# Kernel tuning notes

Measured on AMD Instinct MI355X. Metric: run time of the kernel, lower is better.

## Reference

```python
import jax, jax.numpy as jnp
import numpy as np

C_IN = 512


def _rms(h, gamma):
    # F.normalize(x, dim=1) * sqrt(C) * gamma  (channel_first, h: [b, c, l])
    c = h.shape[1]
    n = jnp.sqrt(jnp.sum(h * h, axis=1, keepdims=True))
    return h / jnp.maximum(n, 1e-12) * (c ** 0.5) * gamma[None, :, None]


def _pw(w, b, h):
    # 1x1 conv == pointwise linear over channel dim; h: [b, c, l]
    return jnp.einsum('oc,bcl->bol', w, h) + b[None, :, None]


def setup_inputs() -> dict:
    key = jax.random.key(0)
    ks = jax.random.split(key, 10)
    B, C, T, H, W = 1, C_IN, 16, 32, 32
    inp = {'x': jax.random.normal(ks[0], (B, C, T, H, W), jnp.float32)}
    names = ['qs', 'ks', 'vs', 'ps', 'qt', 'kt', 'vt', 'pt']
    for i, n in enumerate(names):
        inp[n + '_w'] = jax.random.normal(ks[i + 1], (C, C), jnp.float32) * 0.02
        inp[n + '_b'] = jnp.zeros((C,), jnp.float32)
    inp['norm_s_gamma'] = jnp.ones((C,), jnp.float32)
    inp['norm_t_gamma'] = jnp.ones((C,), jnp.float32)
    inp['max_temporal_window'] = 8
    return inp


def reference(x, qs_w, qs_b, ks_w, ks_b, vs_w, vs_b, ps_w, ps_b,
              qt_w, qt_b, kt_w, kt_b, vt_w, vt_b, pt_w, pt_b,
              norm_s_gamma, norm_t_gamma, max_temporal_window):
    B, C, T, H, W = x.shape
    scale = C ** -0.5

    # ---- spatial attention: (b t) c (h w) ----
    xs = x.transpose(0, 2, 1, 3, 4).reshape(B * T, C, H * W)
    h = _rms(xs, norm_s_gamma)
    q = _pw(qs_w, qs_b, h)
    k = _pw(ks_w, ks_b, h)
    v = _pw(vs_w, vs_b, h)
    scores = jnp.einsum('bcl,bcm->blm', q, k) * scale  # [bt, HW, HW]
    attn = jax.nn.softmax(scores, axis=-1)
    o = jnp.einsum('bcm,blm->bcl', v, attn)
    xs = xs + _pw(ps_w, ps_b, o)
    x = xs.reshape(B, T, C, H, W).transpose(0, 2, 1, 3, 4)

    # ---- temporal attention: (b h w) c t, causal + bounded window ----
    xt = x.transpose(0, 3, 4, 1, 2).reshape(B * H * W, C, T)
    h = _rms(xt, norm_t_gamma)
    q = _pw(qt_w, qt_b, h)
    k = _pw(kt_w, kt_b, h)
    v = _pw(vt_w, vt_b, h)
    scores = jnp.einsum('bcl,bcm->blm', q, k) * scale  # [bhw, T, T]
    i = jnp.arange(T)[:, None]
    j = jnp.arange(T)[None, :]
    allowed = j <= i  # causal
    if max_temporal_window is not None and max_temporal_window > 0:
        allowed = allowed & (i - j < max_temporal_window)  # sliding window
    mask = jnp.where(allowed, 0.0, jnp.finfo(scores.dtype).min)
    attn = jax.nn.softmax(scores + mask[None], axis=-1)
    o = jnp.einsum('bcm,blm->bcl', v, attn)
    xt = xt + _pw(pt_w, pt_b, o)
    x = xt.reshape(B, H, W, C, T).transpose(0, 3, 4, 1, 2)
    return x
```

## Files before the change

### kernel.cpp

```cpp
#include <hip/hip_runtime.h>

typedef __attribute__((ext_vector_type(8))) short bf16x8;
typedef __attribute__((ext_vector_type(4))) float f32x4;

__device__ __forceinline__ short f2bf(float f) {
  union { float f; unsigned u; } a; a.f = f;
  unsigned r = a.u + 0x7fffu + ((a.u >> 16) & 1u);
  return (short)(r >> 16);
}
__device__ __forceinline__ float bf2f(short s) {
  union { unsigned u; float f; } a;
  a.u = ((unsigned)(unsigned short)s) << 16; return a.f;
}
__device__ __forceinline__ float blo(unsigned u) { union { unsigned u; float f; } a; a.u = u << 16; return a.f; }
__device__ __forceinline__ float bhi(unsigned u) { union { unsigned u; float f; } a; a.u = u & 0xffff0000u; return a.f; }
__device__ __forceinline__ unsigned packbf(float lo, float hi) {
  return (unsigned)(unsigned short)f2bf(lo) | ((unsigned)(unsigned short)f2bf(hi) << 16);
}
__device__ __forceinline__ void ldscp16(const void* g, void* l) {
  __builtin_amdgcn_global_load_lds((const __attribute__((address_space(1))) void*)g,
                                   (__attribute__((address_space(3))) void*)l, 16, 0, 0);
}
__device__ __forceinline__ void stv(float* p, float v) { *p = v; }
__device__ __forceinline__ void stv(short* p, float v) { *p = f2bf(v); }

__global__ __launch_bounds__(256) void setup_all(
    const float* __restrict__ w0, const float* __restrict__ w1,
    const float* __restrict__ w2, const float* __restrict__ w3,
    const float* __restrict__ w4, const float* __restrict__ w5,
    const float* __restrict__ w6, const float* __restrict__ w7,
    const float* __restrict__ g_s, const float* __restrict__ g_t,
    short* __restrict__ Wb,
    const float* __restrict__ b0, const float* __restrict__ b1,
    const float* __restrict__ b2, const float* __restrict__ b3,
    const float* __restrict__ b4, const float* __restrict__ b5,
    const float* __restrict__ b6, const float* __restrict__ b7,
    float* __restrict__ Ball, float* __restrict__ zs,
    const float* __restrict__ ps_w, const float* __restrict__ vs_b,
    const float* __restrict__ ps_b, const float* __restrict__ pt_w,
    const float* __restrict__ vt_b, const float* __restrict__ pt_b,
    float* __restrict__ bt_s, float* __restrict__ bt_t) {
  const int bid = blockIdx.x, tid = threadIdx.x;
  if (bid < 8192) {
    int idx = bid * 256 + tid;
    const float* ws[8] = {w0, w1, w2, w3, w4, w5, w6, w7};
    int wi = idx >> 18, loc = idx & 262143;
    int r = loc >> 9, q = loc & 511;
    float v, g;
    if (wi == 2 || wi == 6) {
      v = ws[wi][q * 512 + r];
      g = (wi == 2) ? g_s[r] : g_t[r];
    } else {
      v = ws[wi][loc];
      g = (wi <= 1) ? g_s[q] : (wi == 4 || wi == 5) ? g_t[q] : 1.f;
    }
    Wb[idx] = f2bf(v * g);
  } else if (bid < 8384) {
    zs[(bid - 8192) * 256 + tid] = 0.f;
  } else if (bid < 8400) {
    int idx = (bid - 8384) * 256 + tid;
    const float* bs[8] = {b0, b1, b2, b3, b4, b5, b6, b7};
    Ball[idx] = bs[idx >> 9][idx & 511];
  } else {
    const int w = tid >> 6, lane = tid & 63;
    const int b = (bid - 8400) * 4 + w;
    const bool sp = b < 512;
    const float* W = sp ? ps_w : pt_w;
    const float* vb = sp ? vs_b : vt_b;
    const float* pb = sp ? ps_b : pt_b;
    float* o = sp ? bt_s : bt_t;
    const int r = b & 511;
    float s = 0.f;
#pragma unroll
    for (int c = lane; c < 512; c += 64) s += W[r * 512 + c] * vb[c];
#pragma unroll
    for (int off = 32; off > 0; off >>= 1) s += __shfl_xor(s, off);
    if (lane == 0) o[r] = s + pb[r];
  }
}

__global__ __launch_bounds__(256) void txp_sumsq(
    const float* __restrict__ src, short* __restrict__ dst,
    short* __restrict__ xb, float* __restrict__ ss) {
  constexpr long N = 16384;
  __shared__ short T[64][66];
  __shared__ float part[16][16][4];
  const int tid = threadIdx.x;
  const long n0 = (long)blockIdx.x * 64;
  const int c0 = blockIdx.y * 64;
  const int n4 = (tid & 15) * 4;
  float s0 = 0.f, s1 = 0.f, s2 = 0.f, s3 = 0.f;
#pragma unroll
  for (int i = 0; i < 4; ++i) {
    int cl = i * 16 + (tid >> 4);
    float4 v = *(const float4*)&src[(long)(c0 + cl) * N + n0 + n4];
    s0 += v.x * v.x; s1 += v.y * v.y; s2 += v.z * v.z; s3 += v.w * v.w;
    short e0 = f2bf(v.x), e1 = f2bf(v.y), e2 = f2bf(v.z), e3 = f2bf(v.w);
    T[n4 + 0][cl] = e0; T[n4 + 1][cl] = e1;
    T[n4 + 2][cl] = e2; T[n4 + 3][cl] = e3;
    uint2 o;
    o.x = (unsigned)(unsigned short)e0 | ((unsigned)(unsigned short)e1 << 16);
    o.y = (unsigned)(unsigned short)e2 | ((unsigned)(unsigned short)e3 << 16);
    *(uint2*)&xb[(long)(c0 + cl) * N + n0 + n4] = o;
  }
  part[tid >> 4][tid & 15][0] = s0; part[tid >> 4][tid & 15][1] = s1;
  part[tid >> 4][tid & 15][2] = s2; part[tid >> 4][tid & 15][3] = s3;
  __syncthreads();
  if (tid < 64) {
    float s = 0.f;
#pragma unroll
    for (int cg = 0; cg < 16; ++cg) s += part[cg][tid >> 2][tid & 3];
    atomicAdd(&ss[n0 + tid], s);
  }
#pragma unroll
  for (int p = 0; p < 4; ++p) {
    int nl = p * 16 + (tid >> 4);
    int cl = (tid & 15) * 4;
    uint2 o;
    o.x = (unsigned)(unsigned short)T[nl][cl] |
          ((unsigned)(unsigned short)T[nl][cl + 1] << 16);
    o.y = (unsigned)(unsigned short)T[nl][cl + 2] |
          ((unsigned)(unsigned short)T[nl][cl + 3] << 16);
    *(uint2*)&dst[(n0 + nl) * 512 + c0 + cl] = o;
  }
}

template <typename OutT, int BIAS_MODE, int SCALE_MODE, int RESID_MODE, int EPI>
__global__ __launch_bounds__(256, 3) void gemm_nt(
    const short* __restrict__ A, const short* __restrict__ B,
    OutT* __restrict__ D, const float* __restrict__ bias,
    const float* __restrict__ ssv, float* __restrict__ rs,
    const float* __restrict__ residf, const short* __restrict__ residb,
    int K, int lda, int ldb, int ldd,
    long aBatch, long bBatch, long dBatch, long sBatch, float scale) {
  __shared__ short As[128 * 64];
  __shared__ short Bs[128 * 64];
  const int tid = threadIdx.x;
  const int bz = blockIdx.z;
  const long i0 = (long)blockIdx.x * 128;
  const long j0 = (long)blockIdx.y * 128;
  const short* Ab = A + bz * aBatch + i0 * lda;
  const short* Bb = B + bz * bBatch + j0 * ldb;
  const int srow = tid >> 3, scol = tid & 7;
  const int lane = tid & 63;
  const int wr = ((tid >> 7) & 1) * 64;
  const int wc = ((tid >> 6) & 1) * 64;
  const int quad = lane >> 4, l15 = lane & 15;

  f32x4 acc[4][4] = {};

  for (int k0 = 0; k0 < K; k0 += 64) {
    __syncthreads();
#pragma unroll
    for (int p = 0; p < 4; ++p) {
      int row = p * 32 + srow;
      int gc = (scol ^ (row & 7)) << 3;
      ldscp16(Ab + (long)row * lda + k0 + gc, &As[p * 2048 + tid * 8]);
    }
#pragma unroll
    for (int p = 0; p < 4; ++p) {
      int row = p * 32 + srow;
      int gc = (scol ^ (row & 7)) << 3;
      ldscp16(Bb + (long)row * ldb + k0 + gc, &Bs[p * 2048 + tid * 8]);
    }
    __syncthreads();
#pragma unroll
    for (int kk = 0; kk < 2; ++kk) {
      bf16x8 af[4], bfr[4];
#pragma unroll
      for (int a = 0; a < 4; ++a) {
        int row = wr + a * 16 + l15;
        int g = kk * 4 + quad;
        af[a] = *(const bf16x8*)&As[row * 64 + ((g ^ (row & 7)) << 3)];
      }
#pragma unroll
      for (int b = 0; b < 4; ++b) {
        int row = wc + b * 16 + l15;
        int g = kk * 4 + quad;
        bfr[b] = *(const bf16x8*)&Bs[row * 64 + ((g ^ (row & 7)) << 3)];
      }
#pragma unroll
      for (int a = 0; a < 4; ++a)
#pragma unroll
        for (int b = 0; b < 4; ++b)
          acc[a][b] = __builtin_amdgcn_mfma_f32_16x16x32_bf16(af[a], bfr[b], acc[a][b], 0, 0, 0);
    }
  }

  const long Doff = bz * dBatch;
#pragma unroll
  for (int a = 0; a < 4; ++a) {
    const int rb = (int)i0 + wr + a * 16 + quad * 4;
    float rsc[4];
    if (SCALE_MODE == 1) {
#pragma unroll
      for (int r = 0; r < 4; ++r)
        rsc[r] = 22.627416997969522f /
                 fmaxf(sqrtf(ssv[bz * sBatch + rb + r]), 1e-12f);
    }
    if (SCALE_MODE == 3) {
#pragma unroll
      for (int r = 0; r < 4; ++r)
        rsc[r] = 1.f / ssv[bz * sBatch + rb + r];
    }
    float rowpart[4] = {0.f, 0.f, 0.f, 0.f};
#pragma unroll
    for (int b = 0; b < 4; ++b) {
      const int cc = (int)j0 + wc + b * 16 + l15;
      float csc = 1.f;
      if (SCALE_MODE == 2)
        csc = 22.627416997969522f /
              fmaxf(sqrtf(ssv[bz * sBatch + cc]), 1e-12f);
      uint2 rtv;
      if (RESID_MODE == 3)
        rtv = *(const uint2*)&residb[(long)cc * 512 + rb];
#pragma unroll
      for (int r = 0; r < 4; ++r) {
        float val = acc[a][b][r] * scale;
        if (EPI == 1) { val = __expf(val); rowpart[r] += val; }
        if (SCALE_MODE == 1 || SCALE_MODE == 3) val *= rsc[r];
        if (SCALE_MODE == 2) val *= csc;
        if (BIAS_MODE == 1) val += bias[rb + r];
        if (BIAS_MODE == 2) val += bias[cc];
        const long off = Doff + (long)(rb + r) * ldd + cc;
        if (RESID_MODE == 1) val += residf[off];
        if (RESID_MODE == 2) val += bf2f(residb[off]);
        if (RESID_MODE == 3) val += bf2f(((const short*)&rtv)[r]);
        stv(D + off, val);
        if (EPI == 2) rowpart[r] += val * val;
      }
    }
    if (EPI) {
#pragma unroll
      for (int r = 0; r < 4; ++r) {
        float s = rowpart[r];
#pragma unroll
        for (int off = 1; off < 16; off <<= 1) s += __shfl_xor(s, off);
        if (l15 == 0) atomicAdd(&rs[bz * sBatch + rb + r], s);
      }
    }
  }
}

__global__ __launch_bounds__(256) void temporal_attn_v4(
    const short* __restrict__ qk, const short* __restrict__ h2,
    const float* __restrict__ ss, const int* __restrict__ wndp,
    short* __restrict__ o, float scale) {
  constexpr int RS = 1032;
  __shared__ short qs[16 * RS];
  __shared__ float Plds[16][17];
  const int tid = threadIdx.x;
  const int w = tid >> 6, lane = tid & 63;
  const int hw = blockIdx.x;
  const int wnd = *wndp;

#pragma unroll
  for (int i = 0; i < 8; ++i) {
    int ci = w * 8 + i;
    int t = ci >> 1, half = ci & 1;
    ldscp16(qk + (long)(t * 1024 + hw) * 1024 + half * 512 + lane * 8,
            &qs[t * RS + half * 512 + lane * 8]);
  }
  const int c0 = lane * 8;
  uint4 vch[16];
#pragma unroll
  for (int tp = 0; tp < 16; ++tp)
    vch[tp] = *(const uint4*)(h2 + (long)(tp * 1024 + hw) * 512 + c0);
  __syncthreads();

  if (w == 0) {
    const int quad = lane >> 4, m = lane & 15;
    const short* rowp = &qs[m * RS + quad * 8];
    f32x4 sacc = {};
#pragma unroll
    for (int s = 0; s < 16; ++s) {
      bf16x8 aq = *(const bf16x8*)(rowp + s * 32);
      bf16x8 bk = *(const bf16x8*)(rowp + 512 + s * 32);
      sacc = __builtin_amdgcn_mfma_f32_16x16x32_bf16(aq, bk, sacc, 0, 0, 0);
    }
    const float rmsm = 22.627416997969522f /
                       fmaxf(sqrtf(ss[m * 1024 + hw]), 1e-12f);
#pragma unroll
    for (int r = 0; r < 4; ++r) {
      const int i = quad * 4 + r;
      const int j = m;
      const bool allowed = (j <= i) && (wnd <= 0 || (i - j) < wnd);
      float val = allowed ? sacc[r] * scale : -1e30f;
      float mx = val;
#pragma unroll
      for (int off = 1; off < 16; off <<= 1) mx = fmaxf(mx, __shfl_xor(mx, off));
      float e = allowed ? __expf(val - mx) : 0.f;
      float sum = e;
#pragma unroll
      for (int off = 1; off < 16; off <<= 1) sum += __shfl_xor(sum, off);
      Plds[i][j] = (e / sum) * rmsm;
    }
  }
  __syncthreads();

#pragma unroll
  for (int r = 0; r < 4; ++r) {
    const int t = w * 4 + r;
    const int tlo = (wnd > 0 && t - wnd + 1 > 0) ? t - wnd + 1 : 0;
    float a0 = 0.f, a1 = 0.f, a2 = 0.f, a3 = 0.f,
          a4 = 0.f, a5 = 0.f, a6 = 0.f, a7 = 0.f;
#pragma unroll
    for (int tp = 0; tp < 16; ++tp) {
      const float p = (tp >= tlo && tp <= t) ? Plds[t][tp] : 0.f;
      const uint4 vv = vch[tp];
      a0 += p * blo(vv.x); a1 += p * bhi(vv.x);
      a2 += p * blo(vv.y); a3 += p * bhi(vv.y);
      a4 += p * blo(vv.z); a5 += p * bhi(vv.z);
      a6 += p * blo(vv.w); a7 += p * bhi(vv.w);
    }
    uint4 ov;
    ov.x = packbf(a0, a1); ov.y = packbf(a2, a3);
    ov.z = packbf(a4, a5); ov.w = packbf(a6, a7);
    *(uint4*)(o + (long)(t * 1024 + hw) * 512 + c0) = ov;
  }
}

extern "C" void kernel_launch(void* const* d_in, const int* in_sizes, int n_in,
                              void* d_out, int out_size, void* d_ws, size_t ws_size,
                              hipStream_t stream) {
  const float* x    = (const float*)d_in[0];
  const float* qs_w = (const float*)d_in[1];
  const float* qs_b = (const float*)d_in[2];
  const float* ks_w = (const float*)d_in[3];
  const float* ks_b = (const float*)d_in[4];
  const float* vs_w = (const float*)d_in[5];
  const float* vs_b = (const float*)d_in[6];
  const float* ps_w = (const float*)d_in[7];
  const float* ps_b = (const float*)d_in[8];
  const float* qt_w = (const float*)d_in[9];
  const float* qt_b = (const float*)d_in[10];
  const float* kt_w = (const float*)d_in[11];
  const float* kt_b = (const float*)d_in[12];
  const float* vt_w = (const float*)d_in[13];
  const float* vt_b = (const float*)d_in[14];
  const float* pt_w = (const float*)d_in[15];
  const float* pt_b = (const float*)d_in[16];
  const float* g_s  = (const float*)d_in[17];
  const float* g_t  = (const float*)d_in[18];
  const int*   wnd  = (const int*)d_in[19];
  float* out = (float*)d_out;

  char* w = (char*)d_ws;
  short* Wb   = (short*)(w);
  float* Ball = (float*)(w + (4L << 20));
  float* ss_s = (float*)(w + (4L << 20) + (64 << 10));
  float* ss_t = (float*)(w + (4L << 20) + (128 << 10));
  float* rsum = (float*)(w + (4L << 20) + (192 << 10));
  float* bt_s = (float*)(w + (4L << 20) + (256 << 10));
  float* bt_t = (float*)(w + (4L << 20) + (260 << 10));
  short* Wpv  = (short*)(w + (4L << 20) + (512 << 10));
  short* hb   = (short*)(w + (6L << 20));
  short* QK   = (short*)(w + (22L << 20));
  short* xb   = (short*)(w + (54L << 20));
  short* oT   = (short*)(w + (70L << 20));
  short* h2   = (short*)(w + (86L << 20));
  short* S    = (short*)(w + (102L << 20));
  (void)in_sizes; (void)n_in; (void)out_size; (void)ws_size;

  const float scale = 0.04419417382415922f;

  setup_all<<<8656, 256, 0, stream>>>(
      qs_w, ks_w, vs_w, ps_w, qt_w, kt_w, vt_w, pt_w, g_s, g_t, Wb,
      qs_b, ks_b, vs_b, ps_b, qt_b, kt_b, vt_b, pt_b, Ball, ss_s,
      ps_w, vs_b, ps_b, pt_w, vt_b, pt_b, bt_s, bt_t);
  gemm_nt<short, 0, 0, 0, 0><<<dim3(4, 4, 2), 256, 0, stream>>>(
      Wb + 3 * 262144, Wb + 2 * 262144, Wpv, nullptr, nullptr, nullptr,
      nullptr, nullptr, 512, 512, 512, 512, 4 * 262144L, 4 * 262144L,
      262144L, 0, 1.f);

  txp_sumsq<<<dim3(256, 8, 1), 256, 0, stream>>>(x, hb, xb, ss_s);
  gemm_nt<short, 2, 1, 0, 0><<<dim3(128, 8, 1), 256, 0, stream>>>(
      hb, Wb, QK, Ball, ss_s, nullptr, nullptr, nullptr,
      512, 512, 512, 1024, 0, 0, 0, 0, 1.f);
  gemm_nt<short, 0, 2, 0, 1><<<dim3(8, 8, 16), 256, 0, stream>>>(
      QK, QK + 512, S, nullptr, ss_s, rsum, nullptr, nullptr,
      512, 1024, 1024, 1024,
      1024L * 1024, 1024L * 1024, 1024L * 1024, 1024, scale);
  gemm_nt<short, 0, 3, 0, 0><<<dim3(8, 4, 16), 256, 0, stream>>>(
      S, xb, oT, nullptr, rsum, nullptr, nullptr, nullptr,
      1024, 1024, 16384, 512,
      1024L * 1024, 1024L, 1024L * 512, 1024, 1.f);
  gemm_nt<short, 2, 0, 2, 2><<<dim3(128, 4, 1), 256, 0, stream>>>(
      oT, Wpv, h2, bt_s, nullptr, ss_t, nullptr, hb,
      512, 512, 512, 512, 0, 0, 0, 0, 1.f);

  gemm_nt<short, 2, 1, 0, 0><<<dim3(128, 8, 1), 256, 0, stream>>>(
      h2, Wb + 4 * 262144, QK, Ball + 2048, ss_t, nullptr, nullptr, nullptr,
      512, 512, 512, 1024, 0, 0, 0, 0, 1.f);
  temporal_attn_v4<<<1024, 256, 0, stream>>>(QK, h2, ss_t, wnd, oT, scale);
  gemm_nt<float, 1, 0, 3, 0><<<dim3(4, 128, 1), 256, 0, stream>>>(
      Wpv + 262144, oT, out, bt_t, nullptr, nullptr, nullptr, h2,
      512, 512, 512, 16384, 0, 0, 0, 0, 1.f);
}
```

Before: 314.8 us.

## Fold Q and K projections into a precomputed Wq^T Wk matrix for both attentions

Rather than projecting Q and K separately (a 1024-wide output GEMM), this precomputes M = Wq^T·Wk and a bias vector Wq^T·bq, then computes T = h·M once (512-wide). Scores are formed as h_i·T_j, with RMS scales and the query-bias term applied in the epilogue; the key-bias term is constant per row and cancels in softmax. Spatial and temporal paths both use this, which halves the projection GEMM width and the QK buffer traffic. It adds a few setup GEMMs and extra atomic reductions (us/ut), and changes bf16 rounding, since M is formed in bf16 and raw x is used as the score operand.

After: 309.7 us. Within noise of the previous version (-1.6%).

```diff
diff --git a/kernel.cpp b/kernel.cpp
--- a/kernel.cpp
+++ b/kernel.cpp
@@ -30,16 +30,12 @@
     const float* __restrict__ w4, const float* __restrict__ w5,
     const float* __restrict__ w6, const float* __restrict__ w7,
     const float* __restrict__ g_s, const float* __restrict__ g_t,
-    short* __restrict__ Wb,
-    const float* __restrict__ b0, const float* __restrict__ b1,
-    const float* __restrict__ b2, const float* __restrict__ b3,
-    const float* __restrict__ b4, const float* __restrict__ b5,
-    const float* __restrict__ b6, const float* __restrict__ b7,
-    float* __restrict__ Ball, float* __restrict__ zs,
-    const float* __restrict__ ps_w, const float* __restrict__ vs_b,
-    const float* __restrict__ ps_b, const float* __restrict__ pt_w,
+    short* __restrict__ Wb, float* __restrict__ zs,
+    const float* __restrict__ qs_b, const float* __restrict__ vs_b,
+    const float* __restrict__ ps_b, const float* __restrict__ qt_b,
     const float* __restrict__ vt_b, const float* __restrict__ pt_b,
-    float* __restrict__ bt_s, float* __restrict__ bt_t) {
+    float* __restrict__ bt_s, float* __restrict__ bt_t,
+    float* __restrict__ wus, float* __restrict__ wut) {
   const int bid = blockIdx.x, tid = threadIdx.x;
   if (bid < 8192) {
     int idx = bid * 256 + tid;
@@ -47,54 +43,64 @@
     int wi = idx >> 18, loc = idx & 262143;
     int r = loc >> 9, q = loc & 511;
     float v, g;
-    if (wi == 2 || wi == 6) {
+    if (wi == 3 || wi == 7) { v = ws[wi][loc]; g = 1.f; }
+    else {
       v = ws[wi][q * 512 + r];
-      g = (wi == 2) ? g_s[r] : g_t[r];
-    } else {
-      v = ws[wi][loc];
-      g = (wi <= 1) ? g_s[q] : (wi == 4 || wi == 5) ? g_t[q] : 1.f;
+      g = (wi <= 2) ? g_s[r] : g_t[r];
     }
     Wb[idx] = f2bf(v * g);
-  } else if (bid < 8384) {
+  } else if (bid < 8512) {
     zs[(bid - 8192) * 256 + tid] = 0.f;
-  } else if (bid < 8400) {
-    int idx = (bid - 8384) * 256 + tid;
-    const float* bs[8] = {b0, b1, b2, b3, b4, b5, b6, b7};
-    Ball[idx] = bs[idx >> 9][idx & 511];
   } else {
     const int w = tid >> 6, lane = tid & 63;
-    const int b = (bid - 8400) * 4 + w;
-    const bool sp = b < 512;
-    const float* W = sp ? ps_w : pt_w;
-    const float* vb = sp ? vs_b : vt_b;
-    const float* pb = sp ? ps_b : pt_b;
-    float* o = sp ? bt_s : bt_t;
-    const int r = b & 511;
+    const int b = (bid - 8512) * 4 + w;
     float s = 0.f;
-#pragma unroll
-    for (int c = lane; c < 512; c += 64) s += W[r * 512 + c] * vb[c];
-#pragma unroll
-    for (int off = 32; off > 0; off >>= 1) s += __shfl_xor(s, off);
-    if (lane == 0) o[r] = s + pb[r];
+    if (b < 1024) {
+      const bool sp = b < 512;
+      const float* W = sp ? w3 : w7;
+      const float* vb = sp ? vs_b : vt_b;
+      const int r = b & 511;
+#pragma unroll
+      for (int c = lane; c < 512; c += 64) s += W[r * 512 + c] * vb[c];
+#pragma unroll
+      for (int off = 32; off > 0; off >>= 1) s += __shfl_xor(s, off);
+      if (lane == 0) (sp ? bt_s : bt_t)[r] = s + (sp ? ps_b : pt_b)[r];
+    } else {
+      const bool sp = b < 1536;
+      const float* W = sp ? w1 : w5;
+      const float* qb = sp ? qs_b : qt_b;
+      const int c = b & 511;
+#pragma unroll
+      for (int o = lane; o < 512; o += 64) s += W[o * 512 + c] * qb[o];
+#pragma unroll
+      for (int off = 32; off > 0; off >>= 1) s += __shfl_xor(s, off);
+      if (lane == 0)
+        (sp ? wus : wut)[c] = s * (sp ? g_s[c] : g_t[c]);
+    }
   }
 }
 
 __global__ __launch_bounds__(256) void txp_sumsq(
     const float* __restrict__ src, short* __restrict__ dst,
-    short* __restrict__ xb, float* __restrict__ ss) {
+    short* __restrict__ xb, float* __restrict__ ss,
+    const float* __restrict__ wu, float* __restrict__ us) {
   constexpr long N = 16384;
   __shared__ short T[64][66];
   __shared__ float part[16][16][4];
+  __shared__ float part2[16][16][4];
   const int tid = threadIdx.x;
   const long n0 = (long)blockIdx.x * 64;
   const int c0 = blockIdx.y * 64;
   const int n4 = (tid & 15) * 4;
   float s0 = 0.f, s1 = 0.f, s2 = 0.f, s3 = 0.f;
+  float u0 = 0.f, u1 = 0.f, u2 = 0.f, u3 = 0.f;
 #pragma unroll
   for (int i = 0; i < 4; ++i) {
     int cl = i * 16 + (tid >> 4);
     float4 v = *(const float4*)&src[(long)(c0 + cl) * N + n0 + n4];
+    float wc = wu[c0 + cl];
     s0 += v.x * v.x; s1 += v.y * v.y; s2 += v.z * v.z; s3 += v.w * v.w;
+    u0 += wc * v.x; u1 += wc * v.y; u2 += wc * v.z; u3 += wc * v.w;
     short e0 = f2bf(v.x), e1 = f2bf(v.y), e2 = f2bf(v.z), e3 = f2bf(v.w);
     T[n4 + 0][cl] = e0; T[n4 + 1][cl] = e1;
     T[n4 + 2][cl] = e2; T[n4 + 3][cl] = e3;
@@ -105,12 +111,18 @@
   }
   part[tid >> 4][tid & 15][0] = s0; part[tid >> 4][tid & 15][1] = s1;
   part[tid >> 4][tid & 15][2] = s2; part[tid >> 4][tid & 15][3] = s3;
+  part2[tid >> 4][tid & 15][0] = u0; part2[tid >> 4][tid & 15][1] = u1;
+  part2[tid >> 4][tid & 15][2] = u2; part2[tid >> 4][tid & 15][3] = u3;
   __syncthreads();
   if (tid < 64) {
-    float s = 0.f;
-#pragma unroll
-    for (int cg = 0; cg < 16; ++cg) s += part[cg][tid >> 2][tid & 3];
+    float s = 0.f, u = 0.f;
+#pragma unroll
+    for (int cg = 0; cg < 16; ++cg) {
+      s += part[cg][tid >> 2][tid & 3];
+      u += part2[cg][tid >> 2][tid & 3];
+    }
     atomicAdd(&ss[n0 + tid], s);
+    atomicAdd(&us[n0 + tid], u);
   }
 #pragma unroll
   for (int p = 0; p < 4; ++p) {
@@ -129,7 +141,9 @@
 __global__ __launch_bounds__(256, 3) void gemm_nt(
     const short* __restrict__ A, const short* __restrict__ B,
     OutT* __restrict__ D, const float* __restrict__ bias,
-    const float* __restrict__ ssv, float* __restrict__ rs,
+    const float* __restrict__ ssv, const float* __restrict__ uvec,
+    float* __restrict__ rs, float* __restrict__ rs2,
+    const float* __restrict__ wvec,
     const float* __restrict__ residf, const short* __restrict__ residb,
     int K, int lda, int ldb, int ldd,
     long aBatch, long bBatch, long dBatch, long sBatch, float scale) {
@@ -192,7 +206,7 @@
   for (int a = 0; a < 4; ++a) {
     const int rb = (int)i0 + wr + a * 16 + quad * 4;
     float rsc[4];
-    if (SCALE_MODE == 1) {
+    if (SCALE_MODE == 1 || SCALE_MODE == 4) {
 #pragma unroll
       for (int r = 0; r < 4; ++r)
         rsc[r] = 22.627416997969522f /
@@ -203,23 +217,32 @@
       for (int r = 0; r < 4; ++r)
         rsc[r] = 1.f / ssv[bz * sBatch + rb + r];
     }
-    float rowpart[4] = {0.f, 0.f, 0.f, 0.f};
+    float rp1[4] = {0.f, 0.f, 0.f, 0.f};
+    float rp2[4] = {0.f, 0.f, 0.f, 0.f};
 #pragma unroll
     for (int b = 0; b < 4; ++b) {
       const int cc = (int)j0 + wc + b * 16 + l15;
-      float csc = 1.f;
-      if (SCALE_MODE == 2)
+      float csc = 1.f, uu = 0.f, wv = 0.f;
+      if (SCALE_MODE == 2 || SCALE_MODE == 4)
         csc = 22.627416997969522f /
               fmaxf(sqrtf(ssv[bz * sBatch + cc]), 1e-12f);
+      if (SCALE_MODE == 4) uu = uvec[bz * sBatch + cc];
+      if (EPI == 3) wv = wvec[cc];
       uint2 rtv;
       if (RESID_MODE == 3)
         rtv = *(const uint2*)&residb[(long)cc * 512 + rb];
 #pragma unroll
       for (int r = 0; r < 4; ++r) {
-        float val = acc[a][b][r] * scale;
-        if (EPI == 1) { val = __expf(val); rowpart[r] += val; }
-        if (SCALE_MODE == 1 || SCALE_MODE == 3) val *= rsc[r];
-        if (SCALE_MODE == 2) val *= csc;
+        float val;
+        if (SCALE_MODE == 4) {
+          val = __expf(scale * csc * (rsc[r] * acc[a][b][r] + uu));
+          rp1[r] += val;
+          val *= csc;
+        } else {
+          val = acc[a][b][r] * scale;
+          if (SCALE_MODE == 1 || SCALE_MODE == 3) val *= rsc[r];
+          if (SCALE_MODE == 2) val *= csc;
+        }
         if (BIAS_MODE == 1) val += bias[rb + r];
         if (BIAS_MODE == 2) val += bias[cc];
         const long off = Doff + (long)(rb + r) * ldd + cc;
@@ -227,27 +250,37 @@
         if (RESID_MODE == 2) val += bf2f(residb[off]);
         if (RESID_MODE == 3) val += bf2f(((const short*)&rtv)[r]);
         stv(D + off, val);
-        if (EPI == 2) rowpart[r] += val * val;
+        if (EPI == 3) { rp1[r] += val * val; rp2[r] += val * wv; }
       }
     }
-    if (EPI) {
+    if (EPI == 1 || EPI == 3) {
 #pragma unroll
       for (int r = 0; r < 4; ++r) {
-        float s = rowpart[r];
+        float s = rp1[r];
 #pragma unroll
         for (int off = 1; off < 16; off <<= 1) s += __shfl_xor(s, off);
         if (l15 == 0) atomicAdd(&rs[bz * sBatch + rb + r], s);
       }
-    }
-  }
-}
-
-__global__ __launch_bounds__(256) void temporal_attn_v4(
-    const short* __restrict__ qk, const short* __restrict__ h2,
-    const float* __restrict__ ss, const int* __restrict__ wndp,
-    short* __restrict__ o, float scale) {
-  constexpr int RS = 1032;
-  __shared__ short qs[16 * RS];
+      if (EPI == 3) {
+#pragma unroll
+        for (int r = 0; r < 4; ++r) {
+          float s = rp2[r];
+#pragma unroll
+          for (int off = 1; off < 16; off <<= 1) s += __shfl_xor(s, off);
+          if (l15 == 0) atomicAdd(&rs2[bz * sBatch + rb + r], s);
+        }
+      }
+    }
+  }
+}
+
+__global__ __launch_bounds__(256) void temporal_attn_v5(
+    const short* __restrict__ h2, const short* __restrict__ Tt,
+    const float* __restrict__ ss, const float* __restrict__ ut,
+    const int* __restrict__ wndp, short* __restrict__ o, float scale) {
+  constexpr int RS = 520;
+  __shared__ short hq[16 * RS];
+  __shared__ short tk[16 * RS];
   __shared__ float Plds[16][17];
   const int tid = threadIdx.x;
   const int w = tid >> 6, lane = tid & 63;
@@ -257,9 +290,11 @@
 #pragma unroll
   for (int i = 0; i < 8; ++i) {
     int ci = w * 8 + i;
-    int t = ci >> 1, half = ci & 1;
-    ldscp16(qk + (long)(t * 1024 + hw) * 1024 + half * 512 + lane * 8,
-            &qs[t * RS + half * 512 + lane * 8]);
+    int t = ci & 15;
+    const short* src = (ci < 16) ? h2 : Tt;
+    short* dst = (ci < 16) ? hq : tk;
+    ldscp16(src + (long)(t * 1024 + hw) * 512 + lane * 8,
+            dst + t * RS + lane * 8);
   }
   const int c0 = lane * 8;
   uint4 vch[16];
@@ -270,22 +305,24 @@
 
   if (w == 0) {
     const int quad = lane >> 4, m = lane & 15;
-    const short* rowp = &qs[m * RS + quad * 8];
     f32x4 sacc = {};
 #pragma unroll
     for (int s = 0; s < 16; ++s) {
-      bf16x8 aq = *(const bf16x8*)(rowp + s * 32);
-      bf16x8 bk = *(const bf16x8*)(rowp + 512 + s * 32);
+      bf16x8 aq = *(const bf16x8*)&hq[m * RS + quad * 8 + s * 32];
+      bf16x8 bk = *(const bf16x8*)&tk[m * RS + quad * 8 + s * 32];
       sacc = __builtin_amdgcn_mfma_f32_16x16x32_bf16(aq, bk, sacc, 0, 0, 0);
     }
-    const float rmsm = 22.627416997969522f /
+    const float rmsj = 22.627416997969522f /
                        fmaxf(sqrtf(ss[m * 1024 + hw]), 1e-12f);
+    const float uj = ut[m * 1024 + hw];
 #pragma unroll
     for (int r = 0; r < 4; ++r) {
       const int i = quad * 4 + r;
       const int j = m;
+      const float rmsi = 22.627416997969522f /
+                         fmaxf(sqrtf(ss[i * 1024 + hw]), 1e-12f);
       const bool allowed = (j <= i) && (wnd <= 0 || (i - j) < wnd);
-      float val = allowed ? sacc[r] * scale : -1e30f;
+      float val = allowed ? scale * (rmsi * rmsj * sacc[r] + rmsj * uj) : -1e30f;
       float mx = val;
 #pragma unroll
       for (int off = 1; off < 16; off <<= 1) mx = fmaxf(mx, __shfl_xor(mx, off));
@@ -293,7 +330,7 @@
       float sum = e;
 #pragma unroll
       for (int off = 1; off < 16; off <<= 1) sum += __shfl_xor(sum, off);
-      Plds[i][j] = (e / sum) * rmsm;
+      Plds[i][j] = (e / sum) * rmsj;
     }
   }
   __syncthreads();
@@ -344,56 +381,64 @@
   const float* g_t  = (const float*)d_in[18];
   const int*   wnd  = (const int*)d_in[19];
   float* out = (float*)d_out;
+  (void)ks_b; (void)kt_b;
 
   char* w = (char*)d_ws;
   short* Wb   = (short*)(w);
-  float* Ball = (float*)(w + (4L << 20));
-  float* ss_s = (float*)(w + (4L << 20) + (64 << 10));
-  float* ss_t = (float*)(w + (4L << 20) + (128 << 10));
-  float* rsum = (float*)(w + (4L << 20) + (192 << 10));
-  float* bt_s = (float*)(w + (4L << 20) + (256 << 10));
-  float* bt_t = (float*)(w + (4L << 20) + (260 << 10));
+  float* ss_s = (float*)(w + (4L << 20));
+  float* ss_t = (float*)(w + (4L << 20) + (64 << 10));
+  float* rsum = (float*)(w + (4L << 20) + (128 << 10));
+  float* us   = (float*)(w + (4L << 20) + (192 << 10));
+  float* ut   = (float*)(w + (4L << 20) + (256 << 10));
+  float* bt_s = (float*)(w + (4L << 20) + (320 << 10));
+  float* bt_t = (float*)(w + (4L << 20) + (324 << 10));
+  float* wus  = (float*)(w + (4L << 20) + (328 << 10));
+  float* wut  = (float*)(w + (4L << 20) + (332 << 10));
   short* Wpv  = (short*)(w + (4L << 20) + (512 << 10));
-  short* hb   = (short*)(w + (6L << 20));
-  short* QK   = (short*)(w + (22L << 20));
-  short* xb   = (short*)(w + (54L << 20));
-  short* oT   = (short*)(w + (70L << 20));
-  short* h2   = (short*)(w + (86L << 20));
-  short* S    = (short*)(w + (102L << 20));
+  short* Mqk  = (short*)(w + (5L << 20) + (512 << 10));
+  short* hb   = (short*)(w + (8L << 20));
+  short* Tb   = (short*)(w + (24L << 20));
+  short* xb   = (short*)(w + (40L << 20));
+  short* oT   = (short*)(w + (56L << 20));
+  short* h2   = (short*)(w + (72L << 20));
+  short* S    = (short*)(w + (88L << 20));
   (void)in_sizes; (void)n_in; (void)out_size; (void)ws_size;
 
   const float scale = 0.04419417382415922f;
 
-  setup_all<<<8656, 256, 0, stream>>>(
-      qs_w, ks_w, vs_w, ps_w, qt_w, kt_w, vt_w, pt_w, g_s, g_t, Wb,
-      qs_b, ks_b, vs_b, ps_b, qt_b, kt_b, vt_b, pt_b, Ball, ss_s,
-      ps_w, vs_b, ps_b, pt_w, vt_b, pt_b, bt_s, bt_t);
+  setup_all<<<9024, 256, 0, stream>>>(
+      qs_w, ks_w, vs_w, ps_w, qt_w, kt_w, vt_w, pt_w, g_s, g_t, Wb, ss_s,
+      qs_b, vs_b, ps_b, qt_b, vt_b, pt_b, bt_s, bt_t, wus, wut);
   gemm_nt<short, 0, 0, 0, 0><<<dim3(4, 4, 2), 256, 0, stream>>>(
       Wb + 3 * 262144, Wb + 2 * 262144, Wpv, nullptr, nullptr, nullptr,
-      nullptr, nullptr, 512, 512, 512, 512, 4 * 262144L, 4 * 262144L,
-      262144L, 0, 1.f);
-
-  txp_sumsq<<<dim3(256, 8, 1), 256, 0, stream>>>(x, hb, xb, ss_s);
-  gemm_nt<short, 2, 1, 0, 0><<<dim3(128, 8, 1), 256, 0, stream>>>(
-      hb, Wb, QK, Ball, ss_s, nullptr, nullptr, nullptr,
-      512, 512, 512, 1024, 0, 0, 0, 0, 1.f);
-  gemm_nt<short, 0, 2, 0, 1><<<dim3(8, 8, 16), 256, 0, stream>>>(
-      QK, QK + 512, S, nullptr, ss_s, rsum, nullptr, nullptr,
-      512, 1024, 1024, 1024,
-      1024L * 1024, 1024L * 1024, 1024L * 1024, 1024, scale);
+      nullptr, nullptr, nullptr, nullptr, nullptr,
+      512, 512, 512, 512, 4 * 262144L, 4 * 262144L, 262144L, 0, 1.f);
+  gemm_nt<short, 0, 0, 0, 0><<<dim3(4, 4, 2), 256, 0, stream>>>(
+      Wb, Wb + 262144, Mqk, nullptr, nullptr, nullptr,
+      nullptr, nullptr, nullptr, nullptr, nullptr,
+      512, 512, 512, 512, 4 * 262144L, 4 * 262144L, 262144L, 0, 1.f);
+
+  txp_sumsq<<<dim3(256, 8, 1), 256, 0, stream>>>(x, hb, xb, ss_s, wus, us);
+  gemm_nt<short, 0, 0, 0, 0><<<dim3(128, 4, 1), 256, 0, stream>>>(
+      hb, Mqk, Tb, nullptr, nullptr, nullptr, nullptr, nullptr, nullptr,
+      nullptr, nullptr, 512, 512, 512, 512, 0, 0, 0, 0, 1.f);
+  gemm_nt<short, 0, 4, 0, 1><<<dim3(8, 8, 16), 256, 0, stream>>>(
+      hb, Tb, S, nullptr, ss_s, us, rsum, nullptr, nullptr, nullptr, nullptr,
+      512, 512, 512, 1024,
+      1024L * 512, 1024L * 512, 1024L * 1024, 1024, scale);
   gemm_nt<short, 0, 3, 0, 0><<<dim3(8, 4, 16), 256, 0, stream>>>(
-      S, xb, oT, nullptr, rsum, nullptr, nullptr, nullptr,
-      1024, 1024, 16384, 512,
+      S, xb, oT, nullptr, rsum, nullptr, nullptr, nullptr, nullptr,
+      nullptr, nullptr, 1024, 1024, 16384, 512,
       1024L * 1024, 1024L, 1024L * 512, 1024, 1.f);
-  gemm_nt<short, 2, 0, 2, 2><<<dim3(128, 4, 1), 256, 0, stream>>>(
-      oT, Wpv, h2, bt_s, nullptr, ss_t, nullptr, hb,
-      512, 512, 512, 512, 0, 0, 0, 0, 1.f);
-
-  gemm_nt<short, 2, 1, 0, 0><<<dim3(128, 8, 1), 256, 0, stream>>>(
-      h2, Wb + 4 * 262144, QK, Ball + 2048, ss_t, nullptr, nullptr, nullptr,
-      512, 512, 512, 1024, 0, 0, 0, 0, 1.f);
-  temporal_attn_v4<<<1024, 256, 0, stream>>>(QK, h2, ss_t, wnd, oT, scale);
+  gemm_nt<short, 2, 0, 2, 3><<<dim3(128, 4, 1), 256, 0, stream>>>(
+      oT, Wpv, h2, bt_s, nullptr, nullptr, ss_t, ut, wut, nullptr, hb,
+      512, 512, 512, 512, 0, 0, 0, 1024, 1.f);
+
+  gemm_nt<short, 0, 0, 0, 0><<<dim3(128, 4, 1), 256, 0, stream>>>(
+      h2, Mqk + 262144, Tb, nullptr, nullptr, nullptr, nullptr, nullptr,
+      nullptr, nullptr, nullptr, 512, 512, 512, 512, 0, 0, 0, 0, 1.f);
+  temporal_attn_v5<<<1024, 256, 0, stream>>>(h2, Tb, ss_t, ut, wnd, oT, scale);
   gemm_nt<float, 1, 0, 3, 0><<<dim3(4, 128, 1), 256, 0, stream>>>(
-      Wpv + 262144, oT, out, bt_t, nullptr, nullptr, nullptr, h2,
-      512, 512, 512, 16384, 0, 0, 0, 0, 1.f);
-}
+      Wpv + 262144, oT, out, bt_t, nullptr, nullptr, nullptr, nullptr,
+      nullptr, nullptr, h2, 512, 512, 512, 16384, 0, 0, 0, 0, 1.f);
+}
```
